# Kernel tuning notes

Hardware: AMD Instinct MI355X
Metric: run time of the kernel (lower is better)

Reference implementation:

```python
import jax, jax.numpy as jnp
import numpy as np

B_, N_, D_ = 8, 1024, 64
H_, DH_ = 4, 16
DI_, DS_, DTR_ = 128, 64, 4
MAXP = 512


def _ln(x, w, b, eps=1e-5):
    m = jnp.mean(x, -1, keepdims=True)
    v = jnp.mean((x - m) ** 2, -1, keepdims=True)
    return (x - m) * jax.lax.rsqrt(v + eps) * w + b


def _attn(x, drop_mask, Wq, Wkv, Wo, bo, rel_emb):
    b, n, d = x.shape
    scale = DH_ ** -0.5
    q = (x @ Wq).reshape(b, n, H_, DH_).transpose(0, 2, 1, 3)
    kv = x @ Wkv
    k = kv[..., :d].reshape(b, n, H_, DH_).transpose(0, 2, 1, 3)
    v = kv[..., d:].reshape(b, n, H_, DH_).transpose(0, 2, 1, 3)
    dots = jnp.einsum('bhid,bhjd->bhij', q, k) * scale
    seq = jnp.arange(n)
    dist = jnp.clip(seq[:, None] - seq[None, :], -MAXP, MAXP) + MAXP
    rpe = rel_emb[dist]  # (n, n, DH_)
    dots = dots + jnp.einsum('bhid,ijd->bhij', q, rpe) * scale
    # stochastic key drop: Bernoulli(0.3) positions get -1e12
    dots = dots + drop_mask.astype(dots.dtype) * (-1e12)
    attn = jax.nn.softmax(dots, axis=-1)
    out = jnp.einsum('bhij,bhjd->bhid', attn, v)
    out = out.transpose(0, 2, 1, 3).reshape(b, n, H_ * DH_)
    return out @ Wo + bo


def _mamba(x, W_in, conv_w, conv_b, W_xproj, W_dt, b_dt, A_log, Dm, W_out):
    b, n, _ = x.shape
    xz = x @ W_in                      # (b, n, 2*DI_)
    u, z = xz[..., :DI_], xz[..., DI_:]
    uc = u.transpose(0, 2, 1)          # (b, DI_, n)
    uc = jax.lax.conv_general_dilated(
        uc, conv_w[:, None, :], (1,), ((3, 0),),
        feature_group_count=DI_, dimension_numbers=('NCH', 'OIH', 'NCH'))
    uc = uc + conv_b[None, :, None]
    u = jax.nn.silu(uc).transpose(0, 2, 1)  # (b, n, DI_)
    xdb = u @ W_xproj                  # (b, n, DTR_+2*DS_)
    dt = jax.nn.softplus(xdb[..., :DTR_] @ W_dt + b_dt)  # (b, n, DI_)
    Bm = xdb[..., DTR_:DTR_ + DS_]
    Cm = xdb[..., DTR_ + DS_:]
    A = -jnp.exp(A_log)                # (DI_, DS_)

    def step(h, inp):
        dt_t, B_t, C_t, u_t = inp      # (b,DI_),(b,DS_),(b,DS_),(b,DI_)
        dA = jnp.exp(dt_t[..., None] * A)
        h = h * dA + (dt_t * u_t)[..., None] * B_t[:, None, :]
        y = jnp.einsum('bds,bs->bd', h, C_t)
        return h, y

    h0 = jnp.zeros((b, DI_, DS_), x.dtype)
    xs = (dt.transpose(1, 0, 2), Bm.transpose(1, 0, 2),
          Cm.transpose(1, 0, 2), u.transpose(1, 0, 2))
    _, ys = jax.lax.scan(step, h0, xs)
    y = ys.transpose(1, 0, 2) + u * Dm
    y = y * jax.nn.silu(z)
    return y @ W_out


def _rmsgn(x, gamma, eps=1e-5, groups=4):
    shp = x.shape
    dpg = shp[-1] // groups
    xg = x.reshape(shp[:-1] + (groups, dpg))
    rms = jnp.sqrt(jnp.sum(xg * xg, -1, keepdims=True)) * (dpg ** -0.5)
    return (xg / (rms + eps)).reshape(shp) * gamma


def _ff1(x, c1_w, c1_b, d1_w, d1_b):
    # SwiGLUConvDeconv1d(64, 256, kernel=4, shift=1); x: (b, s2, 64)
    s2 = x.shape[1]
    xc = x.transpose(0, 2, 1)
    xc = jnp.pad(xc, ((0, 0), (0, 0), (3, 3)))
    xc = jax.lax.conv_general_dilated(
        xc, c1_w, (1,), 'VALID', dimension_numbers=('NCH', 'OIH', 'NCH'))
    xc = xc + c1_b[None, :, None]
    gate = jax.nn.silu(xc[:, 256:, :])
    xc = xc[:, :256, :] * gate
    # ConvTranspose1d stride 1 == conv with flipped kernel, full padding
    w = jnp.flip(d1_w, -1).transpose(1, 0, 2)  # (64, 256, 4)
    xc = jax.lax.conv_general_dilated(
        xc, w, (1,), ((3, 3),), dimension_numbers=('NCH', 'OIH', 'NCH'))
    xc = xc + d1_b[None, :, None]
    out = xc.transpose(0, 2, 1)
    return out[:, 3:3 + s2, :]


def _forward(x, drop_mask, ln1_w, ln1_b, Wq, Wkv, Wo, bo, rel_emb,
             ln2_w, ln2_b, W_in, conv_w, conv_b, W_xproj, W_dt, b_dt,
             A_log, Dm, W_out, gamma, c1_w, c1_b, d1_w, d1_b, ln3_w, ln3_b):
    xt = _ln(x, ln1_w, ln1_b)
    xt = _attn(xt, drop_mask, Wq, Wkv, Wo, bo, rel_emb) + x
    x = x + xt  # dropout p=0 -> identity (faithful to original residual math)
    xt = _ln(x, ln2_w, ln2_b)
    m = _mamba(xt, W_in, conv_w, conv_b, W_xproj, W_dt, b_dt, A_log, Dm, W_out)
    m = jnp.where(m >= 0, m, 0.01 * m)  # leaky_relu
    m = _rmsgn(m, gamma)
    m = m + 0.5 * _ff1(m, c1_w, c1_b, d1_w, d1_b)
    x = x + m
    return _ln(x, ln3_w, ln3_b)


def setup_inputs() -> dict:
    ks = jax.random.split(jax.random.key(0), 16)
    g = lambda i, shp, s: jax.random.normal(ks[i], shp, dtype=jnp.float32) * s
    A_log = jnp.log(jnp.tile(jnp.arange(1, DS_ + 1, dtype=jnp.float32)[None, :], (DI_, 1)))
    return {
        'x': jax.random.normal(ks[0], (B_, N_, D_), dtype=jnp.float32),
        'drop_mask': jax.random.bernoulli(ks[1], 0.3, (B_, H_, N_, N_)),
        'ln1_w': jnp.ones((D_,), jnp.float32), 'ln1_b': jnp.zeros((D_,), jnp.float32),
        'Wq': g(2, (D_, D_), 0.1), 'Wkv': g(3, (D_, 2 * D_), 0.1),
        'Wo': g(4, (D_, D_), 0.1), 'bo': jnp.zeros((D_,), jnp.float32),
        'rel_emb': g(5, (2 * MAXP + 1, DH_), 0.02),
        'ln2_w': jnp.ones((D_,), jnp.float32), 'ln2_b': jnp.zeros((D_,), jnp.float32),
        'W_in': g(6, (D_, 2 * DI_), 0.1),
        'conv_w': g(7, (DI_, 4), 0.2), 'conv_b': jnp.zeros((DI_,), jnp.float32),
        'W_xproj': g(8, (DI_, DTR_ + 2 * DS_), 0.1),
        'W_dt': g(9, (DTR_, DI_), 0.1), 'b_dt': jnp.zeros((DI_,), jnp.float32),
        'A_log': A_log, 'Dm': jnp.ones((DI_,), jnp.float32),
        'W_out': g(10, (DI_, D_), 0.1),
        'gamma': jnp.ones((D_,), jnp.float32),
        'c1_w': g(11, (512, 64, 4), 0.1), 'c1_b': jnp.zeros((512,), jnp.float32),
        'd1_w': g(12, (256, 64, 4), 0.1), 'd1_b': jnp.zeros((64,), jnp.float32),
        'ln3_w': jnp.ones((D_,), jnp.float32), 'ln3_b': jnp.zeros((D_,), jnp.float32),
    }


def reference(x, drop_mask, ln1_w, ln1_b, Wq, Wkv, Wo, bo, rel_emb,
              ln2_w, ln2_b, W_in, conv_w, conv_b, W_xproj, W_dt, b_dt,
              A_log, Dm, W_out, gamma, c1_w, c1_b, d1_w, d1_b, ln3_w, ln3_b):
    return _forward(x, drop_mask, ln1_w, ln1_b, Wq, Wkv, Wo, bo, rel_emb,
                    ln2_w, ln2_b, W_in, conv_w, conv_b, W_xproj, W_dt, b_dt,
                    A_log, Dm, W_out, gamma, c1_w, c1_b, d1_w, d1_b, ln3_w, ln3_b)
```

## Files before the change

### kernel.cpp

```cpp
#include <hip/hip_runtime.h>
#include <hip/hip_fp16.h>
#include <math.h>


__device__ __forceinline__ float wsum64(float v){
#pragma unroll
  for(int m=32;m>0;m>>=1) v += __shfl_xor(v, m, 64);
  return v;
}
__device__ __forceinline__ float wmax64(float v){
#pragma unroll
  for(int m=32;m>0;m>>=1) v = fmaxf(v, __shfl_xor(v, m, 64));
  return v;
}
__device__ __forceinline__ float silu_f(float x){ return x / (1.f + __expf(-x)); }
__device__ __forceinline__ float rfl_f(float x){
  return __int_as_float(__builtin_amdgcn_readfirstlane(__float_as_int(x)));
}

__global__ __launch_bounds__(256) void k_ln1_qkv(
    const float* __restrict__ x, const float* __restrict__ w1, const float* __restrict__ b1,
    const float* __restrict__ Wq, const float* __restrict__ Wkv,
    const float* __restrict__ rel, const float* __restrict__ c1w,
    const int* __restrict__ dmask,
    float* __restrict__ qb, float2* __restrict__ kvT,
    float* __restrict__ relT, float* __restrict__ c1wT,
    unsigned long long* __restrict__ mask64, unsigned* __restrict__ KmaxSq){
  int tid = threadIdx.x;
  int bi = blockIdx.x >> 1;
  if (blockIdx.x & 1){
    size_t base = (size_t)bi * 16384;
    const int4* dp4 = (const int4*)(dmask + base);
    unsigned long long* mp = mask64 + (base >> 6);
    int lane = tid & 63, wv = tid >> 6;
    int li = (lane & 15) * 4;
#pragma unroll 1
    for(int p=0; p<4; ++p){
      int4 v0 = dp4[p*1024 + tid*4 + 0];
      int4 v1 = dp4[p*1024 + tid*4 + 1];
      int4 v2 = dp4[p*1024 + tid*4 + 2];
      int4 v3 = dp4[p*1024 + tid*4 + 3];
      unsigned m = 0;
      m |= (v0.x!=0) ? 1u<<0  : 0u;  m |= (v0.y!=0) ? 1u<<1  : 0u;
      m |= (v0.z!=0) ? 1u<<2  : 0u;  m |= (v0.w!=0) ? 1u<<3  : 0u;
      m |= (v1.x!=0) ? 1u<<4  : 0u;  m |= (v1.y!=0) ? 1u<<5  : 0u;
      m |= (v1.z!=0) ? 1u<<6  : 0u;  m |= (v1.w!=0) ? 1u<<7  : 0u;
      m |= (v2.x!=0) ? 1u<<8  : 0u;  m |= (v2.y!=0) ? 1u<<9  : 0u;
      m |= (v2.z!=0) ? 1u<<10 : 0u;  m |= (v2.w!=0) ? 1u<<11 : 0u;
      m |= (v3.x!=0) ? 1u<<12 : 0u;  m |= (v3.y!=0) ? 1u<<13 : 0u;
      m |= (v3.z!=0) ? 1u<<14 : 0u;  m |= (v3.w!=0) ? 1u<<15 : 0u;
      unsigned s0 = __shfl(m, li+0, 64);
      unsigned s1 = __shfl(m, li+1, 64);
      unsigned s2 = __shfl(m, li+2, 64);
      unsigned s3 = __shfl(m, li+3, 64);
      if (lane < 16){
        unsigned long long word = (unsigned long long)s0
          | ((unsigned long long)s1 << 16)
          | ((unsigned long long)s2 << 32)
          | ((unsigned long long)s3 << 48);
        mp[p*64 + wv*16 + lane] = word;
      }
    }
    return;
  }
  int lane = tid & 63, warp = tid >> 6;
  int token = bi*4 + warp;
  __shared__ float xt[4][64];
  float xv = x[(size_t)token*64 + lane];
  float mean = wsum64(xv) * 0.015625f;
  float dlt = xv - mean;
  float var = wsum64(dlt*dlt) * 0.015625f;
  float xn = dlt * rsqrtf(var + 1e-5f) * w1[lane] + b1[lane];
  xt[warp][lane] = xn;
  __syncthreads();
  float aq=0.f, ak=0.f, av=0.f;
#pragma unroll 4
  for(int dd=0; dd<64; ++dd){
    float xd = xt[warp][dd];
    aq += xd * Wq[dd*64 + lane];
    ak += xd * Wkv[dd*128 + lane];
    av += xd * Wkv[dd*128 + 64 + lane];
  }
  int b = token >> 10, i = token & 1023;
  int h = lane >> 4, dh = lane & 15;
  size_t o  = (((size_t)(b*4 + h))*1024 + i)*16 + dh;
  size_t oT = (((size_t)(b*4 + h))*16 + dh)*1024 + i;
  qb[o]=aq;
  kvT[oT] = make_float2(ak, av);

  float kk = ak*ak;
  kk += __shfl_xor(kk, 1, 64);
  kk += __shfl_xor(kk, 2, 64);
  kk += __shfl_xor(kk, 4, 64);
  kk += __shfl_xor(kk, 8, 64);
  if (dh == 0) atomicMax(KmaxSq + (b*4 + h), __float_as_uint(kk));

  if (bi < 65){
    int idx = bi*256 + tid;
    if (idx < 16*1025){
      int c = idx / 1025;
      int d = idx - c*1025;
      relT[idx] = rel[d*16 + c];
    }
  } else if (bi < 577){
    int idx = (bi-65)*256 + tid;
    int row = idx >> 9;
    int ii  = idx & 511;
    c1wT[idx] = c1w[(size_t)ii*256 + row];
  }
}

__global__ __launch_bounds__(256, 2) void k_attn(
    const float* __restrict__ qb, const float2* __restrict__ kvT,
    const unsigned long long* __restrict__ mask64, const float* __restrict__ relT,
    const unsigned* __restrict__ KmaxSq, float* __restrict__ attn_raw){
  int tid = threadIdx.x;
  int lane = tid & 63;
  int wvu  = __builtin_amdgcn_readfirstlane(tid >> 6);
  int wg   = blockIdx.x;
  int xcd  = wg & 7;
  int slot = wg >> 3;
  int bh   = xcd*4 + (slot >> 6);
  int i0   = (slot & 63) * 16;
  int b = bh >> 2, h = bh & 3;
  int R0 = wvu*4, R1 = R0+1, R2 = R0+2, R3 = R0+3;

  __shared__ __align__(16) __half Gc[16][1040];
  __shared__ float kvX[2][16][64];
  __shared__ float kvY[2][16][64];
  __shared__ float qs[16][16];
  __shared__ float G0s[16], G1024s[16];
  __shared__ float gmS[16];
  __shared__ float Ms[16];
  __shared__ float sums[16];

  {
    int r = tid >> 4, c = tid & 15;
    qs[r][c] = qb[((size_t)bh*1024 + i0 + r)*16 + c] * 0.25f;
  }
  __syncthreads();

  float q0[16], q1[16], q2[16], q3[16];
#pragma unroll
  for(int c=0;c<16;++c){
    q0[c]=rfl_f(qs[R0][c]); q1[c]=rfl_f(qs[R1][c]);
    q2[c]=rfl_f(qs[R2][c]); q3[c]=rfl_f(qs[R3][c]);
  }

  const float2* kvb = kvT + (size_t)bh*16*1024;
  float2 st[4];
#define LOADREGS(CH) do{ int _j0=(CH)*64;                                   \
    _Pragma("unroll")                                                       \
    for(int k=0;k<4;++k){ int idx=tid+256*k; int c=idx>>6, jl=idx&63;       \
      st[k]=kvb[c*1024 + _j0 + jl]; } }while(0)
#define WRITEB(NB) do{                                                      \
    _Pragma("unroll")                                                       \
    for(int k=0;k<4;++k){ int idx=tid+256*k; int c=idx>>6, jl=idx&63;       \
      kvX[NB][c][jl]=st[k].x; kvY[NB][c][jl]=st[k].y; } }while(0)
#define LBAR() do{                                                          \
    asm volatile("s_waitcnt lgkmcnt(0)" ::: "memory");                      \
    __builtin_amdgcn_s_barrier();                                           \
    asm volatile("" ::: "memory"); }while(0)

  LOADREGS(0);

#pragma unroll 1
  for(int bb=0; bb<17; ++bb){
    int d = lane + 64*bb;
    if (d <= 1024){
      float rl[16];
#pragma unroll
      for(int c=0;c<16;++c) rl[c] = relT[c*1025 + d];
      float g0=0.f, g1=0.f, g2=0.f, g3=0.f;
#pragma unroll
      for(int c=0;c<16;++c){
        float rc = rl[c];
        g0 += q0[c]*rc; g1 += q1[c]*rc; g2 += q2[c]*rc; g3 += q3[c]*rc;
      }
      if (d == 0){ G0s[R0]=g0; G0s[R1]=g1; G0s[R2]=g2; G0s[R3]=g3; }
      else if (d == 1024){ G1024s[R0]=g0; G1024s[R1]=g1; G1024s[R2]=g2; G1024s[R3]=g3; }
      else {
        int base = i0 + 512 - d;
        int j0r = base + R0;
        if (j0r+0 >= 0 && j0r+0 < 1024) Gc[R0][j0r+0] = __float2half_rn(g0);
        if (j0r+1 >= 0 && j0r+1 < 1024) Gc[R1][j0r+1] = __float2half_rn(g1);
        if (j0r+2 >= 0 && j0r+2 < 1024) Gc[R2][j0r+2] = __float2half_rn(g2);
        if (j0r+3 >= 0 && j0r+3 < 1024) Gc[R3][j0r+3] = __float2half_rn(g3);
      }
    }
  }
  __syncthreads();
  {
    const unsigned long long* mrow = mask64 + ((size_t)bh*1024 + i0)*16;
#pragma unroll 1
    for(int r=0;r<16;++r){
      float g0 = G0s[r], g1 = G1024s[r];
      int lo = i0 + r - 512;
      int hi = i0 + r + 512;
#pragma unroll
      for(int p=0;p<4;++p){
        int j = tid + 256*p;
        unsigned long long w = mrow[r*16 + (j>>6)];
        float g;
        if (j >= hi) g = g0;
        else if (j <= lo) g = g1;
        else g = __half2float(Gc[r][j]);
        if ((w >> (j & 63)) & 1ULL) g = -60000.f;
        Gc[r][j] = __float2half_rn(g);
      }
    }
  }
  __syncthreads();
  {
    int r = tid >> 4, l4 = tid & 15;
    float gm = -3.0e38f;
#pragma unroll
    for(int k=0;k<64;++k) gm = fmaxf(gm, __half2float(Gc[r][l4 + 16*k]));
#pragma unroll
    for(int m=1;m<16;m<<=1) gm = fmaxf(gm, __shfl_xor(gm, m, 64));
    if (l4 == 0) gmS[r] = gm;
  }
  __syncthreads();
  if (tid < 16){
    float qn = 0.f;
#pragma unroll
    for(int c=0;c<16;++c) qn += qs[tid][c]*qs[tid][c];
    float km = sqrtf(__uint_as_float(KmaxSq[bh]));
    Ms[tid] = gmS[tid] + sqrtf(qn)*km;
  }
  __syncthreads();

  float M0 = rfl_f(Ms[R0]), M1 = rfl_f(Ms[R1]);
  float M2 = rfl_f(Ms[R2]), M3 = rfl_f(Ms[R3]);

  float s0=0.f, s1=0.f, s2=0.f, s3=0.f;
  float a0[16], a1[16], a2[16], a3[16];
#pragma unroll
  for(int c=0;c<16;++c){ a0[c]=0.f; a1[c]=0.f; a2[c]=0.f; a3[c]=0.f; }

  WRITEB(0);
  LOADREGS(1);
  LBAR();
  int cur = 0;

#pragma unroll 1
  for(int ch=0; ch<16; ++ch){
    int j = ch*64 + lane;
    float sv0 = __half2float(Gc[R0][j]), sv1 = __half2float(Gc[R1][j]);
    float sv2 = __half2float(Gc[R2][j]), sv3 = __half2float(Gc[R3][j]);
#pragma unroll
    for(int c=0;c<16;++c){
      float kxc = kvX[cur][c][lane];
      sv0 += q0[c]*kxc; sv1 += q1[c]*kxc; sv2 += q2[c]*kxc; sv3 += q3[c]*kxc;
    }
    float p0 = __expf(sv0 - M0), p1 = __expf(sv1 - M1);
    float p2 = __expf(sv2 - M2), p3 = __expf(sv3 - M3);
    s0 += p0; s1 += p1; s2 += p2; s3 += p3;
#pragma unroll
    for(int c=0;c<16;++c){
      float vyc = kvY[cur][c][lane];
      a0[c] += p0*vyc; a1[c] += p1*vyc; a2[c] += p2*vyc; a3[c] += p3*vyc;
    }
    if (ch < 15){
      WRITEB(cur^1);
      if (ch < 14) LOADREGS(ch+2);
    }
    LBAR();
    cur ^= 1;
  }
#undef LOADREGS
#undef WRITEB
#undef LBAR

  s0 = wsum64(s0); s1 = wsum64(s1); s2 = wsum64(s2); s3 = wsum64(s3);
#pragma unroll
  for(int c=0;c<16;++c){
    float x0 = a0[c]; x0 += __shfl_xor(x0,32,64); x0 += __shfl_xor(x0,16,64); a0[c] = x0;
    float x1 = a1[c]; x1 += __shfl_xor(x1,32,64); x1 += __shfl_xor(x1,16,64); a1[c] = x1;
    float x2 = a2[c]; x2 += __shfl_xor(x2,32,64); x2 += __shfl_xor(x2,16,64); a2[c] = x2;
    float x3 = a3[c]; x3 += __shfl_xor(x3,32,64); x3 += __shfl_xor(x3,16,64); a3[c] = x3;
  }
  __syncthreads();
  float* red = (float*)&Gc[0][0];
  if (lane < 16){
#pragma unroll
    for(int c=0;c<16;++c){
      red[R0*272 + lane*17 + c] = a0[c];
      red[R1*272 + lane*17 + c] = a1[c];
      red[R2*272 + lane*17 + c] = a2[c];
      red[R3*272 + lane*17 + c] = a3[c];
    }
  }
  if (lane == 0){ sums[R0]=s0; sums[R1]=s1; sums[R2]=s2; sums[R3]=s3; }
  __syncthreads();
  {
    int row = tid >> 4, c = tid & 15;
    float tot = 0.f;
#pragma unroll
    for(int g=0; g<16; ++g) tot += red[row*272 + g*17 + c];
    attn_raw[((size_t)b*1024 + i0 + row)*64 + h*16 + c] = tot / sums[row];
  }
}

__global__ __launch_bounds__(256) void k_post_attn(
    const float* __restrict__ x, const float* __restrict__ attn_raw,
    const float* __restrict__ Wo, const float* __restrict__ bo,
    const float* __restrict__ ln2w, const float* __restrict__ ln2b,
    const float* __restrict__ W_in,
    float* __restrict__ x2, float* __restrict__ u0, float* __restrict__ zsarr){
  int tid = threadIdx.x;
  int lane = tid & 63, wv = tid >> 6;
  int tok0 = blockIdx.x * 16;
  __shared__ float arS[16][64];
  __shared__ float lnS[16][64];
  for(int l = tid; l < 1024; l += 256)
    arS[l >> 6][l & 63] = attn_raw[(size_t)tok0*64 + l];
  __syncthreads();
#pragma unroll 1
  for(int tt = 0; tt < 4; ++tt){
    int tl = wv*4 + tt;
    int token = tok0 + tl;
    float acc = bo[lane];
#pragma unroll 4
    for(int dd = 0; dd < 64; ++dd) acc += arS[tl][dd] * Wo[dd*64 + lane];
    float t = 2.f*x[(size_t)token*64 + lane] + acc;
    x2[(size_t)token*64 + lane] = t;
    float mean = wsum64(t)*0.015625f;
    float dlt = t - mean;
    float var = wsum64(dlt*dlt)*0.015625f;
    lnS[tl][lane] = dlt*rsqrtf(var+1e-5f)*ln2w[lane] + ln2b[lane];
  }
  __syncthreads();
  int oc = tid;
  float w[64];
#pragma unroll
  for(int dd = 0; dd < 64; ++dd) w[dd] = W_in[dd*256 + oc];
  const float4* lnS4 = (const float4*)&lnS[0][0];
#pragma unroll 1
  for(int tl = 0; tl < 16; ++tl){
    float acc = 0.f;
#pragma unroll
    for(int d4 = 0; d4 < 16; ++d4){
      float4 l4 = lnS4[tl*16 + d4];
      acc += l4.x*w[4*d4] + l4.y*w[4*d4+1] + l4.z*w[4*d4+2] + l4.w*w[4*d4+3];
    }
    int token = tok0 + tl;
    if (oc < 128) u0[(size_t)token*128 + oc] = acc;
    else          zsarr[(size_t)token*128 + (oc-128)] = silu_f(acc);
  }
}

__global__ __launch_bounds__(256) void k_conv_proj(
    const float* __restrict__ u0, const float* __restrict__ conv_w, const float* __restrict__ conv_b,
    const float* __restrict__ W_xproj, const float* __restrict__ W_dt, const float* __restrict__ b_dt,
    float* __restrict__ uarr, float* __restrict__ Bmp, float* __restrict__ Cmp, float* __restrict__ dtarr){
  int sub = threadIdx.x >> 7, c = threadIdx.x & 127;
  int token = blockIdx.x*2 + sub;
  int b = token >> 10, i = token & 1023;
  __shared__ float us[2][128];
  __shared__ float dtin[2][4];
  float acc = conv_b[c];
#pragma unroll
  for(int k2=0;k2<4;++k2){
    int t2 = i - 3 + k2;
    if (t2 >= 0) acc += u0[((size_t)b*1024 + t2)*128 + c]*conv_w[c*4+k2];
  }
  float uv = silu_f(acc);
  uarr[(size_t)token*128 + c] = uv;
  us[sub][c] = uv;
  __syncthreads();
  float accA = 0.f, accB = 0.f;
  int cB = 128 + (c & 3);
#pragma unroll 4
  for(int dd=0; dd<128; ++dd){
    float xd = us[sub][dd];
    accA += xd * W_xproj[dd*132 + c];
    accB += xd * W_xproj[dd*132 + cB];
  }
  if (c < 4){ dtin[sub][c] = accA; Cmp[(size_t)token*64 + 60 + c] = accB; }
  else if (c < 68) Bmp[(size_t)token*64 + (c-4)] = accA;
  else             Cmp[(size_t)token*64 + (c-68)] = accA;
  __syncthreads();
  float dv = b_dt[c];
#pragma unroll
  for(int r2=0;r2<4;++r2) dv += dtin[sub][r2]*W_dt[r2*128 + c];
  dv = fmaxf(dv, 0.f) + log1pf(expf(-fabsf(dv)));
  dtarr[(size_t)token*128 + c] = dv;
}

__global__ __launch_bounds__(256) void k_scan_a(
    const float* __restrict__ dtarr, const float* __restrict__ uarr,
    const float* __restrict__ Bmp, const float* __restrict__ A_log,
    float* __restrict__ Parr, float* __restrict__ Rarr){
  int lane = threadIdx.x & 63, warp = threadIdx.x >> 6;
  int wgid = blockIdx.x;
  int b = wgid & 7;
  int slot = wgid >> 3;
  int d = slot & 127;
  int c = (slot >> 7)*4 + warp;
  size_t pw = (size_t)b*1024 + d*8 + c;
  float A = -expf(A_log[d*64 + lane]);
  int tb = c*128;
  const float* dtp = dtarr + ((size_t)b*1024 + tb)*128 + d;
  const float* up  = uarr  + ((size_t)b*1024 + tb)*128 + d;
  const float* Bp  = Bmp   + ((size_t)b*1024 + tb)*64 + lane;
  float R = 0.f, sdt = 0.f;
  for(int t0=0; t0<128; t0+=8){
    float dtc[8], uc[8], Bc[8];
#pragma unroll
    for(int r=0;r<8;++r){
      dtc[r]=dtp[(size_t)(t0+r)*128]; uc[r]=up[(size_t)(t0+r)*128]; Bc[r]=Bp[(size_t)(t0+r)*64];
    }
#pragma unroll
    for(int r=0;r<8;++r){
      float dt = dtc[r];
      R = R*__expf(dt*A) + dt*uc[r]*Bc[r];
      sdt += dt;
    }
  }
  Parr[pw*64 + lane] = __expf(sdt*A);
  Rarr[pw*64 + lane] = R;
}

__global__ __launch_bounds__(256) void k_scan_c(
    const float* __restrict__ dtarr, const float* __restrict__ uarr,
    const float* __restrict__ Bmp, const float* __restrict__ Cmp,
    const float* __restrict__ zsarr, const float* __restrict__ A_log,
    const float* __restrict__ Dm, const float* __restrict__ Parr,
    const float* __restrict__ Rarr, float* __restrict__ ymp){
  int lane = threadIdx.x & 63, warp = threadIdx.x >> 6;
  int wgid = blockIdx.x;
  int b = wgid & 7;
  int slot = wgid >> 3;
  int d = slot & 127;
  int c = (slot >> 7)*4 + warp;
  size_t pbase = (size_t)b*1024 + d*8;
  float A = -expf(A_log[d*64 + lane]);
  float Dv = Dm[d];
  float h = 0.f;
#pragma unroll 1
  for(int cp=0; cp<c; ++cp){
    float P = Parr[(pbase+cp)*64 + lane];
    float R = Rarr[(pbase+cp)*64 + lane];
    h = h*P + R;
  }
  int tb = c*128;
  const float* dtp = dtarr + ((size_t)b*1024 + tb)*128 + d;
  const float* up  = uarr  + ((size_t)b*1024 + tb)*128 + d;
  const float* zp  = zsarr + ((size_t)b*1024 + tb)*128 + d;
  const float* Bp  = Bmp   + ((size_t)b*1024 + tb)*64 + lane;
  const float* Cp  = Cmp   + ((size_t)b*1024 + tb)*64 + lane;
  float* yp        = ymp   + ((size_t)b*1024 + tb)*128 + d;
  for(int t0=0; t0<128; t0+=8){
    float dtc[8], uc[8], Bc[8], Cc[8], zc[8];
#pragma unroll
    for(int r=0;r<8;++r){
      dtc[r]=dtp[(size_t)(t0+r)*128]; uc[r]=up[(size_t)(t0+r)*128];
      Bc[r]=Bp[(size_t)(t0+r)*64];    Cc[r]=Cp[(size_t)(t0+r)*64];
      zc[r]=zp[(size_t)(t0+r)*128];
    }
    float hc[8];
#pragma unroll
    for(int r=0;r<8;++r){
      float dt = dtc[r];
      h = h*__expf(dt*A) + dt*uc[r]*Bc[r];
      hc[r] = h*Cc[r];
    }
    float y[8];
#pragma unroll
    for(int r=0;r<8;++r) y[r] = wsum64(hc[r]);
    if (lane==0){
#pragma unroll
      for(int r=0;r<8;++r) yp[(size_t)(t0+r)*128] = (y[r] + uc[r]*Dv)*zc[r];
    }
  }
}

__global__ __launch_bounds__(256) void k_wout(
    const float* __restrict__ ymp, const float* __restrict__ W_out,
    const float* __restrict__ gamma, float* __restrict__ marr){
  int lane = threadIdx.x & 63, warp = threadIdx.x >> 6;
  int token = blockIdx.x*4 + warp;
  __shared__ float ys[4][128];
  ys[warp][lane]      = ymp[(size_t)token*128 + lane];
  ys[warp][lane+64]   = ymp[(size_t)token*128 + 64 + lane];
  __syncthreads();
  float acc = 0.f;
#pragma unroll 4
  for(int dd=0; dd<128; ++dd) acc += ys[warp][dd]*W_out[dd*64 + lane];
  acc = acc >= 0.f ? acc : 0.01f*acc;
  float ss = acc*acc;
#pragma unroll
  for(int m=1;m<16;m<<=1) ss += __shfl_xor(ss, m, 64);
  float rms = sqrtf(ss)*0.25f;
  marr[(size_t)token*64 + lane] = acc/(rms + 1e-5f)*gamma[lane];
}

__global__ __launch_bounds__(256) void k_h2(
    const float* __restrict__ marr, const float* __restrict__ c1wT,
    const float* __restrict__ c1b, float* __restrict__ h2){
  int b = blockIdx.y;
  int t0 = blockIdx.x * 16;
  int tid = threadIdx.x;
  __shared__ float ms[19][64];
  for(int l = tid; l < 19*64; l += 256){
    int row = l >> 6, cc = l & 63;
    int t = t0 - 3 + row;
    ms[row][cc] = (t >= 0 && t < 1024) ? marr[((size_t)b*1024 + t)*64 + cc] : 0.f;
  }
  __syncthreads();
  int i = tid;
  float acc1[16], acc2[16];
#pragma unroll
  for(int tl=0;tl<16;++tl){ acc1[tl]=0.f; acc2[tl]=0.f; }
  for(int cc=0; cc<64; ++cc){
    float mv[19];
#pragma unroll
    for(int r2=0;r2<19;++r2) mv[r2] = ms[r2][cc];
    const float* wr = c1wT + (size_t)cc*4*512;
    float wa0 = wr[      i], wa1 = wr[ 512+i], wa2 = wr[1024+i], wa3 = wr[1536+i];
    float wg0 = wr[  256+i], wg1 = wr[ 768+i], wg2 = wr[1280+i], wg3 = wr[1792+i];
#pragma unroll
    for(int tl=0; tl<16; ++tl){
      acc1[tl] += wa0*mv[tl+0] + wa1*mv[tl+1] + wa2*mv[tl+2] + wa3*mv[tl+3];
      acc2[tl] += wg0*mv[tl+0] + wg1*mv[tl+1] + wg2*mv[tl+2] + wg3*mv[tl+3];
    }
  }
  float bb1 = c1b[i], bb2 = c1b[i+256];
#pragma unroll
  for(int tl=0; tl<16; ++tl){
    int t = t0 + tl;
    if (t < 1027){
      float o1 = acc1[tl] + bb1;
      float o2 = acc2[tl] + bb2;
      h2[((size_t)b*1027 + t)*256 + i] = o1 * silu_f(o2);
    }
  }
}

__global__ __launch_bounds__(256) void k_ff_final(
    const float* __restrict__ h2, const float* __restrict__ d1w, const float* __restrict__ d1b,
    const float* __restrict__ x2, const float* __restrict__ marr,
    const float* __restrict__ ln3w, const float* __restrict__ ln3b,
    float* __restrict__ out){
  int b = blockIdx.y;
  int s0 = blockIdx.x * 16;
  int tid = threadIdx.x;
  int o = tid & 63, sg = tid >> 6;
  __shared__ float hs[19][256];
  for(int l = tid; l < 19*256; l += 256){
    int row = l >> 8, cc = l & 255;
    hs[row][cc] = h2[((size_t)b*1027 + s0 + row)*256 + cc];
  }
  __syncthreads();
  int sl = sg*4;
  float acc0=0.f, acc1=0.f, acc2=0.f, acc3=0.f;
  const float4* wb = (const float4*)d1w + o;
#pragma unroll 2
  for(int i2=0; i2<256; ++i2){
    float4 wv = wb[(size_t)i2*64];
    float h0=hs[sl+0][i2], h1=hs[sl+1][i2], h2v=hs[sl+2][i2], h3=hs[sl+3][i2];
    float h4=hs[sl+4][i2], h5=hs[sl+5][i2], h6=hs[sl+6][i2];
    acc0 += h0*wv.w + h1*wv.z + h2v*wv.y + h3*wv.x;
    acc1 += h1*wv.w + h2v*wv.z + h3*wv.y + h4*wv.x;
    acc2 += h2v*wv.w + h3*wv.z + h4*wv.y + h5*wv.x;
    acc3 += h3*wv.w + h4*wv.z + h5*wv.y + h6*wv.x;
  }
  float accs[4] = {acc0, acc1, acc2, acc3};
  float bo_ = d1b[o];
#pragma unroll
  for(int r=0;r<4;++r){
    int s = s0 + sl + r;
    size_t idx = ((size_t)b*1024 + s)*64 + o;
    float tot = x2[idx] + marr[idx] + 0.5f*(accs[r] + bo_);
    float mean = wsum64(tot)*0.015625f;
    float dlt = tot - mean;
    float var = wsum64(dlt*dlt)*0.015625f;
    out[idx] = dlt*rsqrtf(var+1e-5f)*ln3w[o] + ln3b[o];
  }
}

extern "C" void kernel_launch(void* const* d_in, const int* in_sizes, int n_in,
                              void* d_out, int out_size, void* d_ws, size_t ws_size,
                              hipStream_t stream){
  const float* x       = (const float*)d_in[0];
  const int*   dmask   = (const int*)  d_in[1];
  const float* ln1w    = (const float*)d_in[2];
  const float* ln1b    = (const float*)d_in[3];
  const float* Wq      = (const float*)d_in[4];
  const float* Wkv     = (const float*)d_in[5];
  const float* Wo      = (const float*)d_in[6];
  const float* bo      = (const float*)d_in[7];
  const float* rel     = (const float*)d_in[8];
  const float* ln2w    = (const float*)d_in[9];
  const float* ln2b    = (const float*)d_in[10];
  const float* W_in    = (const float*)d_in[11];
  const float* conv_w  = (const float*)d_in[12];
  const float* conv_b  = (const float*)d_in[13];
  const float* W_xproj = (const float*)d_in[14];
  const float* W_dt    = (const float*)d_in[15];
  const float* b_dt    = (const float*)d_in[16];
  const float* A_log   = (const float*)d_in[17];
  const float* Dm      = (const float*)d_in[18];
  const float* W_out   = (const float*)d_in[19];
  const float* gamma   = (const float*)d_in[20];
  const float* c1w     = (const float*)d_in[21];
  const float* c1b     = (const float*)d_in[22];
  const float* d1w     = (const float*)d_in[23];
  const float* d1b     = (const float*)d_in[24];
  const float* ln3w    = (const float*)d_in[25];
  const float* ln3b    = (const float*)d_in[26];
  float* outp = (float*)d_out;

  float* ws = (float*)d_ws;
  float* qb       = ws;
  float* kvT      = qb      + 524288;
  float* attn_raw = kvT     + 1048576;
  float* x2       = attn_raw+ 524288;
  float* u0       = x2      + 524288;
  float* zsarr    = u0      + 1048576;
  float* uarr     = zsarr   + 1048576;
  float* dtarr    = uarr    + 1048576;
  float* Bmp      = dtarr   + 1048576;
  float* Cmp      = Bmp     + 524288;
  float* ymp      = Cmp     + 524288;
  float* marr     = ymp     + 1048576;
  float* h2       = marr    + 524288;
  float* relT     = h2      + 2103296;
  float* c1wT     = relT    + 16400;
  float* Parr     = c1wT    + 131072;
  float* Rarr     = Parr    + 524288;
  float* Kmaxa    = Rarr    + 524288;

  unsigned long long* mask64 = (unsigned long long*)h2;
  unsigned* KmaxSqU = (unsigned*)Kmaxa;

  hipMemsetAsync(KmaxSqU, 0, 32*sizeof(unsigned), stream);
  k_ln1_qkv  <<<4096, 256, 0, stream>>>(x, ln1w, ln1b, Wq, Wkv, rel, c1w, dmask,
                                        qb, (float2*)kvT, relT, c1wT, mask64, KmaxSqU);
  k_attn     <<<2048, 256, 0, stream>>>(qb, (const float2*)kvT, mask64, relT, KmaxSqU, attn_raw);
  k_post_attn<<<512, 256, 0, stream>>>(x, attn_raw, Wo, bo, ln2w, ln2b, W_in, x2, u0, zsarr);
  k_conv_proj<<<4096, 256, 0, stream>>>(u0, conv_w, conv_b, W_xproj, W_dt, b_dt, uarr, Bmp, Cmp, dtarr);
  k_scan_a   <<<2048, 256, 0, stream>>>(dtarr, uarr, Bmp, A_log, Parr, Rarr);
  k_scan_c   <<<2048, 256, 0, stream>>>(dtarr, uarr, Bmp, Cmp, zsarr, A_log, Dm, Parr, Rarr, ymp);
  k_wout     <<<2048, 256, 0, stream>>>(ymp, W_out, gamma, marr);
  k_h2       <<<dim3(65,8), 256, 0, stream>>>(marr, c1wT, c1b, h2);
  k_ff_final <<<dim3(64,8), 256, 0, stream>>>(h2, d1w, d1b, x2, marr, ln3w, ln3b, outp);
}
```

Baseline: 717.2 us.

## Widen attention blocks to 512 threads and fuse two-pass scan into one kernel

The attention kernel now runs 512 threads per block with 8 waves each handling 2 query rows instead of 4. This cuts per-thread registers and raises occupancy, with launch bounds set to 3 blocks. The two scan kernels are merged into one: 8 waves per block each compute a chunk's carry, exchange it through shared memory, then do the second pass. This removes a launch and the global round trip for the carries, at the cost of redundant chunk recomputation disappearing but fewer blocks (1024) for the scan.

```diff
diff --git a/kernel.cpp b/kernel.cpp
--- a/kernel.cpp
+++ b/kernel.cpp
@@ -110,7 +110,7 @@
   }
 }
 
-__global__ __launch_bounds__(256, 2) void k_attn(
+__global__ __launch_bounds__(512, 3) void k_attn(
     const float* __restrict__ qb, const float2* __restrict__ kvT,
     const unsigned long long* __restrict__ mask64, const float* __restrict__ relT,
     const unsigned* __restrict__ KmaxSq, float* __restrict__ attn_raw){
@@ -123,7 +123,7 @@
   int bh   = xcd*4 + (slot >> 6);
   int i0   = (slot & 63) * 16;
   int b = bh >> 2, h = bh & 3;
-  int R0 = wvu*4, R1 = R0+1, R2 = R0+2, R3 = R0+3;
+  int R0 = wvu*2, R1 = R0+1;
 
   __shared__ __align__(16) __half Gc[16][1040];
   __shared__ float kvX[2][16][64];
@@ -134,28 +134,27 @@
   __shared__ float Ms[16];
   __shared__ float sums[16];
 
-  {
+  if (tid < 256){
     int r = tid >> 4, c = tid & 15;
     qs[r][c] = qb[((size_t)bh*1024 + i0 + r)*16 + c] * 0.25f;
   }
   __syncthreads();
 
-  float q0[16], q1[16], q2[16], q3[16];
+  float q0[16], q1[16];
 #pragma unroll
   for(int c=0;c<16;++c){
     q0[c]=rfl_f(qs[R0][c]); q1[c]=rfl_f(qs[R1][c]);
-    q2[c]=rfl_f(qs[R2][c]); q3[c]=rfl_f(qs[R3][c]);
   }
 
   const float2* kvb = kvT + (size_t)bh*16*1024;
-  float2 st[4];
+  float2 st[2];
 #define LOADREGS(CH) do{ int _j0=(CH)*64;                                   \
     _Pragma("unroll")                                                       \
-    for(int k=0;k<4;++k){ int idx=tid+256*k; int c=idx>>6, jl=idx&63;       \
+    for(int k=0;k<2;++k){ int idx=tid+512*k; int c=idx>>6, jl=idx&63;       \
       st[k]=kvb[c*1024 + _j0 + jl]; } }while(0)
 #define WRITEB(NB) do{                                                      \
     _Pragma("unroll")                                                       \
-    for(int k=0;k<4;++k){ int idx=tid+256*k; int c=idx>>6, jl=idx&63;       \
+    for(int k=0;k<2;++k){ int idx=tid+512*k; int c=idx>>6, jl=idx&63;       \
       kvX[NB][c][jl]=st[k].x; kvY[NB][c][jl]=st[k].y; } }while(0)
 #define LBAR() do{                                                          \
     asm volatile("s_waitcnt lgkmcnt(0)" ::: "memory");                      \
@@ -171,21 +170,18 @@
       float rl[16];
 #pragma unroll
       for(int c=0;c<16;++c) rl[c] = relT[c*1025 + d];
-      float g0=0.f, g1=0.f, g2=0.f, g3=0.f;
+      float g0=0.f, g1=0.f;
 #pragma unroll
       for(int c=0;c<16;++c){
         float rc = rl[c];
-        g0 += q0[c]*rc; g1 += q1[c]*rc; g2 += q2[c]*rc; g3 += q3[c]*rc;
+        g0 += q0[c]*rc; g1 += q1[c]*rc;
       }
-      if (d == 0){ G0s[R0]=g0; G0s[R1]=g1; G0s[R2]=g2; G0s[R3]=g3; }
-      else if (d == 1024){ G1024s[R0]=g0; G1024s[R1]=g1; G1024s[R2]=g2; G1024s[R3]=g3; }
+      if (d == 0){ G0s[R0]=g0; G0s[R1]=g1; }
+      else if (d == 1024){ G1024s[R0]=g0; G1024s[R1]=g1; }
       else {
-        int base = i0 + 512 - d;
-        int j0r = base + R0;
+        int j0r = i0 + 512 - d + R0;
         if (j0r+0 >= 0 && j0r+0 < 1024) Gc[R0][j0r+0] = __float2half_rn(g0);
         if (j0r+1 >= 0 && j0r+1 < 1024) Gc[R1][j0r+1] = __float2half_rn(g1);
-        if (j0r+2 >= 0 && j0r+2 < 1024) Gc[R2][j0r+2] = __float2half_rn(g2);
-        if (j0r+3 >= 0 && j0r+3 < 1024) Gc[R3][j0r+3] = __float2half_rn(g3);
       }
     }
   }
@@ -198,8 +194,8 @@
       int lo = i0 + r - 512;
       int hi = i0 + r + 512;
 #pragma unroll
-      for(int p=0;p<4;++p){
-        int j = tid + 256*p;
+      for(int p=0;p<2;++p){
+        int j = tid + 512*p;
         unsigned long long w = mrow[r*16 + (j>>6)];
         float g;
         if (j >= hi) g = g0;
@@ -212,13 +208,13 @@
   }
   __syncthreads();
   {
-    int r = tid >> 4, l4 = tid & 15;
+    int r = tid >> 5, l5 = tid & 31;
     float gm = -3.0e38f;
 #pragma unroll
-    for(int k=0;k<64;++k) gm = fmaxf(gm, __half2float(Gc[r][l4 + 16*k]));
-#pragma unroll
-    for(int m=1;m<16;m<<=1) gm = fmaxf(gm, __shfl_xor(gm, m, 64));
-    if (l4 == 0) gmS[r] = gm;
+    for(int k=0;k<32;++k) gm = fmaxf(gm, __half2float(Gc[r][l5 + 32*k]));
+#pragma unroll
+    for(int m=1;m<32;m<<=1) gm = fmaxf(gm, __shfl_xor(gm, m, 64));
+    if ((lane&31) == 0) gmS[r] = gm;
   }
   __syncthreads();
   if (tid < 16){
@@ -231,12 +227,11 @@
   __syncthreads();
 
   float M0 = rfl_f(Ms[R0]), M1 = rfl_f(Ms[R1]);
-  float M2 = rfl_f(Ms[R2]), M3 = rfl_f(Ms[R3]);
-
-  float s0=0.f, s1=0.f, s2=0.f, s3=0.f;
-  float a0[16], a1[16], a2[16], a3[16];
-#pragma unroll
-  for(int c=0;c<16;++c){ a0[c]=0.f; a1[c]=0.f; a2[c]=0.f; a3[c]=0.f; }
+
+  float s0=0.f, s1=0.f;
+  float a0[16], a1[16];
+#pragma unroll
+  for(int c=0;c<16;++c){ a0[c]=0.f; a1[c]=0.f; }
 
   WRITEB(0);
   LOADREGS(1);
@@ -247,19 +242,17 @@
   for(int ch=0; ch<16; ++ch){
     int j = ch*64 + lane;
     float sv0 = __half2float(Gc[R0][j]), sv1 = __half2float(Gc[R1][j]);
-    float sv2 = __half2float(Gc[R2][j]), sv3 = __half2float(Gc[R3][j]);
 #pragma unroll
     for(int c=0;c<16;++c){
       float kxc = kvX[cur][c][lane];
-      sv0 += q0[c]*kxc; sv1 += q1[c]*kxc; sv2 += q2[c]*kxc; sv3 += q3[c]*kxc;
+      sv0 += q0[c]*kxc; sv1 += q1[c]*kxc;
     }
     float p0 = __expf(sv0 - M0), p1 = __expf(sv1 - M1);
-    float p2 = __expf(sv2 - M2), p3 = __expf(sv3 - M3);
-    s0 += p0; s1 += p1; s2 += p2; s3 += p3;
+    s0 += p0; s1 += p1;
 #pragma unroll
     for(int c=0;c<16;++c){
       float vyc = kvY[cur][c][lane];
-      a0[c] += p0*vyc; a1[c] += p1*vyc; a2[c] += p2*vyc; a3[c] += p3*vyc;
+      a0[c] += p0*vyc; a1[c] += p1*vyc;
     }
     if (ch < 15){
       WRITEB(cur^1);
@@ -272,13 +265,11 @@
 #undef WRITEB
 #undef LBAR
 
-  s0 = wsum64(s0); s1 = wsum64(s1); s2 = wsum64(s2); s3 = wsum64(s3);
+  s0 = wsum64(s0); s1 = wsum64(s1);
 #pragma unroll
   for(int c=0;c<16;++c){
     float x0 = a0[c]; x0 += __shfl_xor(x0,32,64); x0 += __shfl_xor(x0,16,64); a0[c] = x0;
     float x1 = a1[c]; x1 += __shfl_xor(x1,32,64); x1 += __shfl_xor(x1,16,64); a1[c] = x1;
-    float x2 = a2[c]; x2 += __shfl_xor(x2,32,64); x2 += __shfl_xor(x2,16,64); a2[c] = x2;
-    float x3 = a3[c]; x3 += __shfl_xor(x3,32,64); x3 += __shfl_xor(x3,16,64); a3[c] = x3;
   }
   __syncthreads();
   float* red = (float*)&Gc[0][0];
@@ -287,13 +278,11 @@
     for(int c=0;c<16;++c){
       red[R0*272 + lane*17 + c] = a0[c];
       red[R1*272 + lane*17 + c] = a1[c];
-      red[R2*272 + lane*17 + c] = a2[c];
-      red[R3*272 + lane*17 + c] = a3[c];
-    }
-  }
-  if (lane == 0){ sums[R0]=s0; sums[R1]=s1; sums[R2]=s2; sums[R3]=s3; }
-  __syncthreads();
-  {
+    }
+  }
+  if (lane == 0){ sums[R0]=s0; sums[R1]=s1; }
+  __syncthreads();
+  if (tid < 256){
     int row = tid >> 4, c = tid & 15;
     float tot = 0.f;
 #pragma unroll
@@ -388,62 +377,18 @@
   dtarr[(size_t)token*128 + c] = dv;
 }
 
-__global__ __launch_bounds__(256) void k_scan_a(
-    const float* __restrict__ dtarr, const float* __restrict__ uarr,
-    const float* __restrict__ Bmp, const float* __restrict__ A_log,
-    float* __restrict__ Parr, float* __restrict__ Rarr){
-  int lane = threadIdx.x & 63, warp = threadIdx.x >> 6;
-  int wgid = blockIdx.x;
-  int b = wgid & 7;
-  int slot = wgid >> 3;
-  int d = slot & 127;
-  int c = (slot >> 7)*4 + warp;
-  size_t pw = (size_t)b*1024 + d*8 + c;
-  float A = -expf(A_log[d*64 + lane]);
-  int tb = c*128;
-  const float* dtp = dtarr + ((size_t)b*1024 + tb)*128 + d;
-  const float* up  = uarr  + ((size_t)b*1024 + tb)*128 + d;
-  const float* Bp  = Bmp   + ((size_t)b*1024 + tb)*64 + lane;
-  float R = 0.f, sdt = 0.f;
-  for(int t0=0; t0<128; t0+=8){
-    float dtc[8], uc[8], Bc[8];
-#pragma unroll
-    for(int r=0;r<8;++r){
-      dtc[r]=dtp[(size_t)(t0+r)*128]; uc[r]=up[(size_t)(t0+r)*128]; Bc[r]=Bp[(size_t)(t0+r)*64];
-    }
-#pragma unroll
-    for(int r=0;r<8;++r){
-      float dt = dtc[r];
-      R = R*__expf(dt*A) + dt*uc[r]*Bc[r];
-      sdt += dt;
-    }
-  }
-  Parr[pw*64 + lane] = __expf(sdt*A);
-  Rarr[pw*64 + lane] = R;
-}
-
-__global__ __launch_bounds__(256) void k_scan_c(
+__global__ __launch_bounds__(512) void k_scan(
     const float* __restrict__ dtarr, const float* __restrict__ uarr,
     const float* __restrict__ Bmp, const float* __restrict__ Cmp,
     const float* __restrict__ zsarr, const float* __restrict__ A_log,
-    const float* __restrict__ Dm, const float* __restrict__ Parr,
-    const float* __restrict__ Rarr, float* __restrict__ ymp){
-  int lane = threadIdx.x & 63, warp = threadIdx.x >> 6;
-  int wgid = blockIdx.x;
-  int b = wgid & 7;
-  int slot = wgid >> 3;
-  int d = slot & 127;
-  int c = (slot >> 7)*4 + warp;
-  size_t pbase = (size_t)b*1024 + d*8;
+    const float* __restrict__ Dm, float* __restrict__ ymp){
+  int lane = threadIdx.x & 63, c = threadIdx.x >> 6;
+  int wg = blockIdx.x;
+  int b = wg & 7;
+  int d = wg >> 3;
+  __shared__ float Ps[8][64], Rs[8][64];
   float A = -expf(A_log[d*64 + lane]);
   float Dv = Dm[d];
-  float h = 0.f;
-#pragma unroll 1
-  for(int cp=0; cp<c; ++cp){
-    float P = Parr[(pbase+cp)*64 + lane];
-    float R = Rarr[(pbase+cp)*64 + lane];
-    h = h*P + R;
-  }
   int tb = c*128;
   const float* dtp = dtarr + ((size_t)b*1024 + tb)*128 + d;
   const float* up  = uarr  + ((size_t)b*1024 + tb)*128 + d;
@@ -451,6 +396,26 @@
   const float* Bp  = Bmp   + ((size_t)b*1024 + tb)*64 + lane;
   const float* Cp  = Cmp   + ((size_t)b*1024 + tb)*64 + lane;
   float* yp        = ymp   + ((size_t)b*1024 + tb)*128 + d;
+  float R = 0.f, sdt = 0.f;
+  for(int t0=0; t0<128; t0+=8){
+    float dtc[8], uc[8], Bc[8];
+#pragma unroll
+    for(int r=0;r<8;++r){
+      dtc[r]=dtp[(size_t)(t0+r)*128]; uc[r]=up[(size_t)(t0+r)*128]; Bc[r]=Bp[(size_t)(t0+r)*64];
+    }
+#pragma unroll
+    for(int r=0;r<8;++r){
+      float dt = dtc[r];
+      R = R*__expf(dt*A) + dt*uc[r]*Bc[r];
+      sdt += dt;
+    }
+  }
+  Ps[c][lane] = __expf(sdt*A);
+  Rs[c][lane] = R;
+  __syncthreads();
+  float h = 0.f;
+#pragma unroll 1
+  for(int cp=0; cp<c; ++cp) h = h*Ps[cp][lane] + Rs[cp][lane];
   for(int t0=0; t0<128; t0+=8){
     float dtc[8], uc[8], Bc[8], Cc[8], zc[8];
 #pragma unroll
@@ -638,11 +603,10 @@
   hipMemsetAsync(KmaxSqU, 0, 32*sizeof(unsigned), stream);
   k_ln1_qkv  <<<4096, 256, 0, stream>>>(x, ln1w, ln1b, Wq, Wkv, rel, c1w, dmask,
                                         qb, (float2*)kvT, relT, c1wT, mask64, KmaxSqU);
-  k_attn     <<<2048, 256, 0, stream>>>(qb, (const float2*)kvT, mask64, relT, KmaxSqU, attn_raw);
+  k_attn     <<<2048, 512, 0, stream>>>(qb, (const float2*)kvT, mask64, relT, KmaxSqU, attn_raw);
   k_post_attn<<<512, 256, 0, stream>>>(x, attn_raw, Wo, bo, ln2w, ln2b, W_in, x2, u0, zsarr);
   k_conv_proj<<<4096, 256, 0, stream>>>(u0, conv_w, conv_b, W_xproj, W_dt, b_dt, uarr, Bmp, Cmp, dtarr);
-  k_scan_a   <<<2048, 256, 0, stream>>>(dtarr, uarr, Bmp, A_log, Parr, Rarr);
-  k_scan_c   <<<2048, 256, 0, stream>>>(dtarr, uarr, Bmp, Cmp, zsarr, A_log, Dm, Parr, Rarr, ymp);
+  k_scan     <<<1024, 512, 0, stream>>>(dtarr, uarr, Bmp, Cmp, zsarr, A_log, Dm, ymp);
   k_wout     <<<2048, 256, 0, stream>>>(ymp, W_out, gamma, marr);
   k_h2       <<<dim3(65,8), 256, 0, stream>>>(marr, c1wT, c1b, h2);
   k_ff_final <<<dim3(64,8), 256, 0, stream>>>(h2, d1w, d1b, x2, marr, ln3w, ln3b, outp);
```

Result: no change. 714.3 us (-0.4%).

## Fuse two-pass chunked scan into one kernel; vectorize attention K/V LDS reads

Applied to the files above, without the earlier changes.

The separate chunk-summary and chunk-apply scan kernels are merged into one 512-thread workgroup per (batch, channel). Each of its 8 waves computes its chunk's decay product and partial state, exchanges them through shared memory, then runs the output pass. This removes one launch and the global round-trip of the P/R arrays, but it cuts the block count and has all chunks synchronize on a barrier. Separately, the attention kernel stores K/V tiles as padded float4 per key so each lane reads four channels with one 128-bit LDS load instead of scalar reads.

```diff
diff --git a/kernel.cpp b/kernel.cpp
--- a/kernel.cpp
+++ b/kernel.cpp
@@ -126,8 +126,8 @@
   int R0 = wvu*4, R1 = R0+1, R2 = R0+2, R3 = R0+3;
 
   __shared__ __align__(16) __half Gc[16][1040];
-  __shared__ float kvX[2][16][64];
-  __shared__ float kvY[2][16][64];
+  __shared__ __align__(16) float4 kX4[2][64][5];
+  __shared__ __align__(16) float4 kV4[2][64][5];
   __shared__ float qs[16][16];
   __shared__ float G0s[16], G1024s[16];
   __shared__ float gmS[16];
@@ -148,15 +148,14 @@
   }
 
   const float2* kvb = kvT + (size_t)bh*16*1024;
+  int jj = tid & 63, cg = tid >> 6;
   float2 st[4];
 #define LOADREGS(CH) do{ int _j0=(CH)*64;                                   \
     _Pragma("unroll")                                                       \
-    for(int k=0;k<4;++k){ int idx=tid+256*k; int c=idx>>6, jl=idx&63;       \
-      st[k]=kvb[c*1024 + _j0 + jl]; } }while(0)
+    for(int i_=0;i_<4;++i_) st[i_]=kvb[(cg*4+i_)*1024 + _j0 + jj]; }while(0)
 #define WRITEB(NB) do{                                                      \
-    _Pragma("unroll")                                                       \
-    for(int k=0;k<4;++k){ int idx=tid+256*k; int c=idx>>6, jl=idx&63;       \
-      kvX[NB][c][jl]=st[k].x; kvY[NB][c][jl]=st[k].y; } }while(0)
+    kX4[NB][jj][cg]=make_float4(st[0].x,st[1].x,st[2].x,st[3].x);           \
+    kV4[NB][jj][cg]=make_float4(st[0].y,st[1].y,st[2].y,st[3].y); }while(0)
 #define LBAR() do{                                                          \
     asm volatile("s_waitcnt lgkmcnt(0)" ::: "memory");                      \
     __builtin_amdgcn_s_barrier();                                           \
@@ -180,8 +179,7 @@
       if (d == 0){ G0s[R0]=g0; G0s[R1]=g1; G0s[R2]=g2; G0s[R3]=g3; }
       else if (d == 1024){ G1024s[R0]=g0; G1024s[R1]=g1; G1024s[R2]=g2; G1024s[R3]=g3; }
       else {
-        int base = i0 + 512 - d;
-        int j0r = base + R0;
+        int j0r = i0 + 512 - d + R0;
         if (j0r+0 >= 0 && j0r+0 < 1024) Gc[R0][j0r+0] = __float2half_rn(g0);
         if (j0r+1 >= 0 && j0r+1 < 1024) Gc[R1][j0r+1] = __float2half_rn(g1);
         if (j0r+2 >= 0 && j0r+2 < 1024) Gc[R2][j0r+2] = __float2half_rn(g2);
@@ -249,17 +247,23 @@
     float sv0 = __half2float(Gc[R0][j]), sv1 = __half2float(Gc[R1][j]);
     float sv2 = __half2float(Gc[R2][j]), sv3 = __half2float(Gc[R3][j]);
 #pragma unroll
-    for(int c=0;c<16;++c){
-      float kxc = kvX[cur][c][lane];
-      sv0 += q0[c]*kxc; sv1 += q1[c]*kxc; sv2 += q2[c]*kxc; sv3 += q3[c]*kxc;
+    for(int c4=0;c4<4;++c4){
+      float4 kx = kX4[cur][lane][c4];
+      sv0 += q0[4*c4+0]*kx.x + q0[4*c4+1]*kx.y + q0[4*c4+2]*kx.z + q0[4*c4+3]*kx.w;
+      sv1 += q1[4*c4+0]*kx.x + q1[4*c4+1]*kx.y + q1[4*c4+2]*kx.z + q1[4*c4+3]*kx.w;
+      sv2 += q2[4*c4+0]*kx.x + q2[4*c4+1]*kx.y + q2[4*c4+2]*kx.z + q2[4*c4+3]*kx.w;
+      sv3 += q3[4*c4+0]*kx.x + q3[4*c4+1]*kx.y + q3[4*c4+2]*kx.z + q3[4*c4+3]*kx.w;
     }
     float p0 = __expf(sv0 - M0), p1 = __expf(sv1 - M1);
     float p2 = __expf(sv2 - M2), p3 = __expf(sv3 - M3);
     s0 += p0; s1 += p1; s2 += p2; s3 += p3;
 #pragma unroll
-    for(int c=0;c<16;++c){
-      float vyc = kvY[cur][c][lane];
-      a0[c] += p0*vyc; a1[c] += p1*vyc; a2[c] += p2*vyc; a3[c] += p3*vyc;
+    for(int c4=0;c4<4;++c4){
+      float4 vy = kV4[cur][lane][c4];
+      a0[4*c4+0] += p0*vy.x; a0[4*c4+1] += p0*vy.y; a0[4*c4+2] += p0*vy.z; a0[4*c4+3] += p0*vy.w;
+      a1[4*c4+0] += p1*vy.x; a1[4*c4+1] += p1*vy.y; a1[4*c4+2] += p1*vy.z; a1[4*c4+3] += p1*vy.w;
+      a2[4*c4+0] += p2*vy.x; a2[4*c4+1] += p2*vy.y; a2[4*c4+2] += p2*vy.z; a2[4*c4+3] += p2*vy.w;
+      a3[4*c4+0] += p3*vy.x; a3[4*c4+1] += p3*vy.y; a3[4*c4+2] += p3*vy.z; a3[4*c4+3] += p3*vy.w;
     }
     if (ch < 15){
       WRITEB(cur^1);
@@ -388,62 +392,18 @@
   dtarr[(size_t)token*128 + c] = dv;
 }
 
-__global__ __launch_bounds__(256) void k_scan_a(
-    const float* __restrict__ dtarr, const float* __restrict__ uarr,
-    const float* __restrict__ Bmp, const float* __restrict__ A_log,
-    float* __restrict__ Parr, float* __restrict__ Rarr){
-  int lane = threadIdx.x & 63, warp = threadIdx.x >> 6;
-  int wgid = blockIdx.x;
-  int b = wgid & 7;
-  int slot = wgid >> 3;
-  int d = slot & 127;
-  int c = (slot >> 7)*4 + warp;
-  size_t pw = (size_t)b*1024 + d*8 + c;
-  float A = -expf(A_log[d*64 + lane]);
-  int tb = c*128;
-  const float* dtp = dtarr + ((size_t)b*1024 + tb)*128 + d;
-  const float* up  = uarr  + ((size_t)b*1024 + tb)*128 + d;
-  const float* Bp  = Bmp   + ((size_t)b*1024 + tb)*64 + lane;
-  float R = 0.f, sdt = 0.f;
-  for(int t0=0; t0<128; t0+=8){
-    float dtc[8], uc[8], Bc[8];
-#pragma unroll
-    for(int r=0;r<8;++r){
-      dtc[r]=dtp[(size_t)(t0+r)*128]; uc[r]=up[(size_t)(t0+r)*128]; Bc[r]=Bp[(size_t)(t0+r)*64];
-    }
-#pragma unroll
-    for(int r=0;r<8;++r){
-      float dt = dtc[r];
-      R = R*__expf(dt*A) + dt*uc[r]*Bc[r];
-      sdt += dt;
-    }
-  }
-  Parr[pw*64 + lane] = __expf(sdt*A);
-  Rarr[pw*64 + lane] = R;
-}
-
-__global__ __launch_bounds__(256) void k_scan_c(
+__global__ __launch_bounds__(512) void k_scan(
     const float* __restrict__ dtarr, const float* __restrict__ uarr,
     const float* __restrict__ Bmp, const float* __restrict__ Cmp,
     const float* __restrict__ zsarr, const float* __restrict__ A_log,
-    const float* __restrict__ Dm, const float* __restrict__ Parr,
-    const float* __restrict__ Rarr, float* __restrict__ ymp){
-  int lane = threadIdx.x & 63, warp = threadIdx.x >> 6;
-  int wgid = blockIdx.x;
-  int b = wgid & 7;
-  int slot = wgid >> 3;
-  int d = slot & 127;
-  int c = (slot >> 7)*4 + warp;
-  size_t pbase = (size_t)b*1024 + d*8;
+    const float* __restrict__ Dm, float* __restrict__ ymp){
+  int lane = threadIdx.x & 63, c = threadIdx.x >> 6;
+  int wg = blockIdx.x;
+  int b = wg & 7;
+  int d = wg >> 3;
+  __shared__ float Ps[8][64], Rs[8][64];
   float A = -expf(A_log[d*64 + lane]);
   float Dv = Dm[d];
-  float h = 0.f;
-#pragma unroll 1
-  for(int cp=0; cp<c; ++cp){
-    float P = Parr[(pbase+cp)*64 + lane];
-    float R = Rarr[(pbase+cp)*64 + lane];
-    h = h*P + R;
-  }
   int tb = c*128;
   const float* dtp = dtarr + ((size_t)b*1024 + tb)*128 + d;
   const float* up  = uarr  + ((size_t)b*1024 + tb)*128 + d;
@@ -451,6 +411,26 @@
   const float* Bp  = Bmp   + ((size_t)b*1024 + tb)*64 + lane;
   const float* Cp  = Cmp   + ((size_t)b*1024 + tb)*64 + lane;
   float* yp        = ymp   + ((size_t)b*1024 + tb)*128 + d;
+  float R = 0.f, sdt = 0.f;
+  for(int t0=0; t0<128; t0+=8){
+    float dtc[8], uc[8], Bc[8];
+#pragma unroll
+    for(int r=0;r<8;++r){
+      dtc[r]=dtp[(size_t)(t0+r)*128]; uc[r]=up[(size_t)(t0+r)*128]; Bc[r]=Bp[(size_t)(t0+r)*64];
+    }
+#pragma unroll
+    for(int r=0;r<8;++r){
+      float dt = dtc[r];
+      R = R*__expf(dt*A) + dt*uc[r]*Bc[r];
+      sdt += dt;
+    }
+  }
+  Ps[c][lane] = __expf(sdt*A);
+  Rs[c][lane] = R;
+  __syncthreads();
+  float h = 0.f;
+#pragma unroll 1
+  for(int cp=0; cp<c; ++cp) h = h*Ps[cp][lane] + Rs[cp][lane];
   for(int t0=0; t0<128; t0+=8){
     float dtc[8], uc[8], Bc[8], Cc[8], zc[8];
 #pragma unroll
@@ -641,8 +621,7 @@
   k_attn     <<<2048, 256, 0, stream>>>(qb, (const float2*)kvT, mask64, relT, KmaxSqU, attn_raw);
   k_post_attn<<<512, 256, 0, stream>>>(x, attn_raw, Wo, bo, ln2w, ln2b, W_in, x2, u0, zsarr);
   k_conv_proj<<<4096, 256, 0, stream>>>(u0, conv_w, conv_b, W_xproj, W_dt, b_dt, uarr, Bmp, Cmp, dtarr);
-  k_scan_a   <<<2048, 256, 0, stream>>>(dtarr, uarr, Bmp, A_log, Parr, Rarr);
-  k_scan_c   <<<2048, 256, 0, stream>>>(dtarr, uarr, Bmp, Cmp, zsarr, A_log, Dm, Parr, Rarr, ymp);
+  k_scan     <<<1024, 512, 0, stream>>>(dtarr, uarr, Bmp, Cmp, zsarr, A_log, Dm, ymp);
   k_wout     <<<2048, 256, 0, stream>>>(ymp, W_out, gamma, marr);
   k_h2       <<<dim3(65,8), 256, 0, stream>>>(marr, c1wT, c1b, h2);
   k_ff_final <<<dim3(64,8), 256, 0, stream>>>(h2, d1w, d1b, x2, marr, ln3w, ln3b, outp);
```

Result: no change. 720.6 us (+0.5%).
